# Performance work log

Hardware: AMD Instinct MI355X
Metric: run time of the kernel (lower is better)

The kernel has to match this reference:

```python
import jax, jax.numpy as jnp
import numpy as np

N = 100000   # nodes
E = 800000   # directed edges (before self-loops)
D = 64       # hidden_dim
NUM_ROUNDS = 4
EPS = 1e-5


def setup_inputs() -> dict:
    key = jax.random.key(0)
    k0, k1, k2 = jax.random.split(key, 3)
    x = jax.random.normal(k0, (N, D), dtype=jnp.float32)
    edge_index = jax.random.randint(k1, (2, E), 0, N, dtype=jnp.int32)
    W = jax.random.normal(k2, (D, D), dtype=jnp.float32) * (1.0 / np.sqrt(D))
    b = jnp.zeros((D,), dtype=jnp.float32)
    gamma = jnp.ones((D,), dtype=jnp.float32)
    beta = jnp.zeros((D,), dtype=jnp.float32)
    return {"x": x, "edge_index": edge_index, "W": W, "b": b,
            "gamma": gamma, "beta": beta, "num_rounds": NUM_ROUNDS}


def reference(x, edge_index, W, b, gamma, beta, num_rounds):
    n = x.shape[0]
    # GCNConv: add self-loops, symmetric degree normalization D^-1/2 (A+I) D^-1/2
    loops = jnp.arange(n, dtype=edge_index.dtype)
    src = jnp.concatenate([edge_index[0], loops])  # [E+N] message sources
    dst = jnp.concatenate([edge_index[1], loops])  # [E+N] message targets
    deg = jax.ops.segment_sum(jnp.ones_like(dst, dtype=x.dtype), dst, num_segments=n)
    dis = jnp.where(deg > 0, jax.lax.rsqrt(deg), 0.0)  # deg^-1/2, 0 for isolated
    norm = dis[src] * dis[dst]                          # [E+N] edge weights

    for _ in range(num_rounds):
        h = x @ W                                                      # [N, D]
        msgs = h[src] * norm[:, None]                                  # gather [E+N, D]
        agg = jax.ops.segment_sum(msgs, dst, num_segments=n) + b      # scatter-add
        # LayerNorm over feature dim
        mu = agg.mean(axis=-1, keepdims=True)
        var = agg.var(axis=-1, keepdims=True)
        x = (agg - mu) * jax.lax.rsqrt(var + EPS) * gamma + beta
    return x
```

## Files before the change

### kernel.cpp

```cpp
#include <hip/hip_runtime.h>

#define D 64
#define EPSV 1e-5f
#define SLOTP 16
#define SLOTS2 24
#define BSH 9
#define BNODES (1 << BSH)
#define BCAP 8192
#define SRCBITS 17
#define SRCMASK ((1u << SRCBITS) - 1)
#define DGSHIFT 26

typedef _Float16 f16;
typedef _Float16 f16x8 __attribute__((ext_vector_type(8)));
typedef float f32x4 __attribute__((ext_vector_type(4)));


__global__ void k_init(int* gcnt, int nbk, const float* __restrict__ W,
                       f16* __restrict__ Wp) {
    const int t = threadIdx.x;
    if (t < nbk) gcnt[t] = 0;
    for (int idx = t; idx < 512; idx += 256) {
        int s = idx >> 8, rem = idx & 255, tt = rem >> 6, l = rem & 63;
        int q = l >> 4, c = l & 15;
#pragma unroll
        for (int j = 0; j < 8; ++j) {
            int k = 32 * s + 8 * q + j;
            Wp[(size_t)idx * 8 + j] = (f16)W[k * D + 16 * tt + c];
        }
    }
}

__global__ __launch_bounds__(256) void k_binA(
    const int* __restrict__ src, const int* __restrict__ dst,
    int* __restrict__ gcnt, unsigned* __restrict__ breg, int e, int nbk) {
    __shared__ int bcnt[256];
    __shared__ int gbase[256];
    const int tid = threadIdx.x;
    if (tid < nbk) bcnt[tid] = 0;
    __syncthreads();

    const int per = (e + gridDim.x - 1) / gridDim.x;
    const int lo = blockIdx.x * per;
    const int hi = min(e, lo + per);

    for (int i = lo + tid; i < hi; i += 256)
        atomicAdd(&bcnt[dst[i] >> BSH], 1);
    __syncthreads();

    if (tid < nbk) {
        int c = bcnt[tid];
        gbase[tid] = (c > 0) ? atomicAdd(&gcnt[tid], c) : 0;
        bcnt[tid] = 0;
    }
    __syncthreads();

    for (int i = lo + tid; i < hi; i += 256) {
        int d_ = dst[i], s_ = src[i];
        int bkt = d_ >> BSH;
        int p = gbase[bkt] + atomicAdd(&bcnt[bkt], 1);
        if (p < BCAP)
            breg[(size_t)bkt * BCAP + p] =
                ((unsigned)(d_ & (BNODES - 1)) << SRCBITS) | (unsigned)s_;
    }
}

__global__ __launch_bounds__(256) void k_binB(
    const int* __restrict__ gcnt, const unsigned* __restrict__ breg,
    unsigned* __restrict__ slots, unsigned* __restrict__ slots2,
    const float* __restrict__ x, const f16* __restrict__ Wp,
    f16* __restrict__ h, int n) {
    __shared__ int scnt[BNODES];
    __shared__ unsigned sbuf[BNODES][SLOTP];
    const int tid = threadIdx.x;
    const int bkt = blockIdx.x;
    const int base = bkt << BSH;
    const int nloc = min(BNODES, n - base);

    for (int i = tid; i < BNODES; i += 256) {
        scnt[i] = 0;
        sbuf[i][0] = 0;
    }
    __syncthreads();

    const int cnt = min(gcnt[bkt], BCAP);
    const unsigned* reg = breg + (size_t)bkt * BCAP;
    for (int i = tid; i < cnt; i += 256) {
        unsigned v = reg[i];
        int ld = v >> SRCBITS;
        unsigned s = v & SRCMASK;
        int p = atomicAdd(&scnt[ld], 1);
        if (p < SLOTP) sbuf[ld][p] = s;
        else if (p < SLOTP + SLOTS2)
            slots2[(size_t)(base + ld) * SLOTS2 + (p - SLOTP)] = s;
    }
    __syncthreads();

    for (int i = tid; i < nloc * 4; i += 256) {
        int ld = i >> 2, part = i & 3;
        uint4 v = ((const uint4*)sbuf[ld])[part];
        if (part == 0) v.x |= (unsigned)min(scnt[ld], 63) << DGSHIFT;
        ((uint4*)(slots + (size_t)(base + ld) * SLOTP))[part] = v;
    }

    const int lane = tid & 63, wv = tid >> 6;
    const int q = lane >> 4, c = lane & 15;
    const f16x8* wp = (const f16x8*)Wp;
    f16x8 w0 = wp[0 * 64 + lane], w1 = wp[1 * 64 + lane];
    f16x8 w2 = wp[2 * 64 + lane], w3 = wp[3 * 64 + lane];
    f16x8 w4 = wp[4 * 64 + lane], w5 = wp[5 * 64 + lane];
    f16x8 w6 = wp[6 * 64 + lane], w7 = wp[7 * 64 + lane];

    for (int t = wv; t < 32; t += 4) {
        const int row0 = base + t * 16;
        if (row0 >= n) break;
        const int rA = (row0 + c < n) ? (row0 + c) : (n - 1);

        const float4* xr = (const float4*)(x + (size_t)rA * D);
        float4 u0 = xr[2 * q], u1 = xr[2 * q + 1];
        float4 u2 = xr[8 + 2 * q], u3 = xr[9 + 2 * q];
        f16x8 a0 = (f16x8){(f16)u0.x, (f16)u0.y, (f16)u0.z, (f16)u0.w,
                           (f16)u1.x, (f16)u1.y, (f16)u1.z, (f16)u1.w};
        f16x8 a1 = (f16x8){(f16)u2.x, (f16)u2.y, (f16)u2.z, (f16)u2.w,
                           (f16)u3.x, (f16)u3.y, (f16)u3.z, (f16)u3.w};

        f32x4 d0 = {0,0,0,0}, d1 = {0,0,0,0}, d2 = {0,0,0,0}, d3 = {0,0,0,0};
        d0 = __builtin_amdgcn_mfma_f32_16x16x32_f16(a0, w0, d0, 0, 0, 0);
        d1 = __builtin_amdgcn_mfma_f32_16x16x32_f16(a0, w1, d1, 0, 0, 0);
        d2 = __builtin_amdgcn_mfma_f32_16x16x32_f16(a0, w2, d2, 0, 0, 0);
        d3 = __builtin_amdgcn_mfma_f32_16x16x32_f16(a0, w3, d3, 0, 0, 0);
        d0 = __builtin_amdgcn_mfma_f32_16x16x32_f16(a1, w4, d0, 0, 0, 0);
        d1 = __builtin_amdgcn_mfma_f32_16x16x32_f16(a1, w5, d1, 0, 0, 0);
        d2 = __builtin_amdgcn_mfma_f32_16x16x32_f16(a1, w6, d2, 0, 0, 0);
        d3 = __builtin_amdgcn_mfma_f32_16x16x32_f16(a1, w7, d3, 0, 0, 0);

#pragma unroll
        for (int r = 0; r < 4; ++r) {
            int row = row0 + q * 4 + r;
            if (row < n) {
                float dvr = rsqrtf((float)(scnt[t * 16 + q * 4 + r] + 1));
                f16* hr = h + (size_t)row * D + c;
                hr[0]  = (f16)(d0[r] * dvr);
                hr[16] = (f16)(d1[r] * dvr);
                hr[32] = (f16)(d2[r] * dvr);
                hr[48] = (f16)(d3[r] * dvr);
            }
        }
    }
}

template<bool LAST>
__global__ __launch_bounds__(256, 8) void k_fuse(
    const f16* __restrict__ h, const unsigned* __restrict__ slots,
    const unsigned* __restrict__ slots2,
    const float* __restrict__ bb, const float* __restrict__ gamma,
    const float* __restrict__ beta, const f16* __restrict__ Wp,
    float* __restrict__ out, f16* __restrict__ hnext, int n,
    int sq, int sr) {
    __shared__ __align__(16) f16 ylds[32][72];
    __shared__ int dgs[32];

    const int xb = blockIdx.x & 7, kb = blockIdx.x >> 3;
    const int bid = (xb < sr ? xb * (sq + 1) : sr * (sq + 1) + (xb - sr) * sq) + kb;

    const int tid = threadIdx.x;
    const int grp = tid >> 3;
    const int fl  = tid & 7;
    const int w = bid * 32 + grp;
    const bool act = (w < n);

    if (act) {
        const int jb = w * SLOTP;

        float acc[8];
        {
            f16x8 sv = *(const f16x8*)(h + (size_t)w * D + fl * 8);
#pragma unroll
            for (int f = 0; f < 8; ++f) acc[f] = (float)sv[f];
        }

        uint4 s0 = *(const uint4*)(slots + jb);
        uint4 s1 = *(const uint4*)(slots + jb + 4);
        uint4 s2 = *(const uint4*)(slots + jb + 8);
        const int dg = (int)(s0.x >> DGSHIFT);
        if (!LAST && fl == 0) dgs[grp] = dg;
        const unsigned idx[12] = {s0.x & SRCMASK, s0.y, s0.z, s0.w,
                                  s1.x, s1.y, s1.z, s1.w,
                                  s2.x, s2.y, s2.z, s2.w};
        f16x8 v[12];
#pragma unroll
        for (int k = 0; k < 12; ++k) {
            unsigned u = (k < dg) ? idx[k] : 0u;
            v[k] = *(const f16x8*)(h + (size_t)u * D + fl * 8);
        }
#pragma unroll
        for (int k = 0; k < 12; ++k) {
            float m = (k < dg) ? 1.0f : 0.0f;
#pragma unroll
            for (int f = 0; f < 8; ++f) acc[f] += m * (float)v[k][f];
        }
        const int dgp = (dg < SLOTP) ? dg : SLOTP;
        if (dgp > 12) {
            uint4 sr4 = *(const uint4*)(slots + jb + 12);
            const unsigned uu[4] = {sr4.x, sr4.y, sr4.z, sr4.w};
#pragma unroll
            for (int k = 0; k < 4; ++k) {
                unsigned u = (12 + k < dgp) ? uu[k] : 0u;
                float m = (12 + k < dgp) ? 1.0f : 0.0f;
                f16x8 vv = *(const f16x8*)(h + (size_t)u * D + fl * 8);
#pragma unroll
                for (int f = 0; f < 8; ++f) acc[f] += m * (float)vv[f];
            }
        }
        if (dg > SLOTP) {
            const unsigned* r2 = slots2 + (size_t)w * SLOTS2;
            int dg2 = dg - SLOTP; if (dg2 > SLOTS2) dg2 = SLOTS2;
#pragma unroll
            for (int base = 0; base < SLOTS2; base += 4) {
                if (base < dg2) {
                    uint4 sr4 = *(const uint4*)(r2 + base);
                    const unsigned uu[4] = {sr4.x, sr4.y, sr4.z, sr4.w};
#pragma unroll
                    for (int k = 0; k < 4; ++k) {
                        unsigned u = (base + k < dg2) ? uu[k] : 0u;
                        float m = (base + k < dg2) ? 1.0f : 0.0f;
                        f16x8 vv = *(const f16x8*)(h + (size_t)u * D + fl * 8);
#pragma unroll
                        for (int f = 0; f < 8; ++f) acc[f] += m * (float)vv[f];
                    }
                }
            }
        }

        const float dv = rsqrtf((float)(dg + 1));
        const float4 b0 = ((const float4*)bb)[fl * 2],    b1 = ((const float4*)bb)[fl * 2 + 1];
        const float4 g0 = ((const float4*)gamma)[fl * 2], g1 = ((const float4*)gamma)[fl * 2 + 1];
        const float4 e0 = ((const float4*)beta)[fl * 2],  e1 = ((const float4*)beta)[fl * 2 + 1];
        const float bs[8] = {b0.x, b0.y, b0.z, b0.w, b1.x, b1.y, b1.z, b1.w};
        const float gs[8] = {g0.x, g0.y, g0.z, g0.w, g1.x, g1.y, g1.z, g1.w};
        const float es[8] = {e0.x, e0.y, e0.z, e0.w, e1.x, e1.y, e1.z, e1.w};

#pragma unroll
        for (int f = 0; f < 8; ++f) acc[f] = acc[f] * dv + bs[f];

        float s = 0.0f;
#pragma unroll
        for (int f = 0; f < 8; ++f) s += acc[f];
#pragma unroll
        for (int m = 1; m < 8; m <<= 1) s += __shfl_xor(s, m);
        float mu = s * (1.0f / 64.0f);
        float dd[8], qv = 0.0f;
#pragma unroll
        for (int f = 0; f < 8; ++f) { dd[f] = acc[f] - mu; qv += dd[f] * dd[f]; }
#pragma unroll
        for (int m = 1; m < 8; m <<= 1) qv += __shfl_xor(qv, m);
        float rstd = rsqrtf(qv * (1.0f / 64.0f) + EPSV);

        if (LAST) {
            float4 o0, o1;
            o0.x = dd[0] * rstd * gs[0] + es[0]; o0.y = dd[1] * rstd * gs[1] + es[1];
            o0.z = dd[2] * rstd * gs[2] + es[2]; o0.w = dd[3] * rstd * gs[3] + es[3];
            o1.x = dd[4] * rstd * gs[4] + es[4]; o1.y = dd[5] * rstd * gs[5] + es[5];
            o1.z = dd[6] * rstd * gs[6] + es[6]; o1.w = dd[7] * rstd * gs[7] + es[7];
            float4* orow = (float4*)(out + (size_t)w * D);
            orow[fl * 2] = o0; orow[fl * 2 + 1] = o1;
        } else {
            f16x8 yv;
#pragma unroll
            for (int f = 0; f < 8; ++f) yv[f] = (f16)(dd[f] * rstd * gs[f] + es[f]);
            *(f16x8*)(&ylds[grp][fl * 8]) = yv;
        }
    }
    if (LAST) return;

    __syncthreads();

    const int wv = tid >> 6;
    const int lane = tid & 63;
    const int q = lane >> 4, c = lane & 15;

    const f16x8* wp = (const f16x8*)Wp;
    f16x8 wlo = wp[wv * 64 + lane];
    f16x8 whi = wp[(4 + wv) * 64 + lane];

    const int row0 = bid * 32;
#pragma unroll
    for (int rt = 0; rt < 2; ++rt) {
        f16x8 a0 = *(const f16x8*)(&ylds[rt * 16 + c][q * 8]);
        f16x8 a1 = *(const f16x8*)(&ylds[rt * 16 + c][32 + q * 8]);
        f32x4 d = {0, 0, 0, 0};
        d = __builtin_amdgcn_mfma_f32_16x16x32_f16(a0, wlo, d, 0, 0, 0);
        d = __builtin_amdgcn_mfma_f32_16x16x32_f16(a1, whi, d, 0, 0, 0);

        const int rbase = row0 + rt * 16;
#pragma unroll
        for (int r = 0; r < 4; ++r) {
            int row = rbase + q * 4 + r;
            if (row < n) {
                float dvr = rsqrtf((float)(dgs[rt * 16 + q * 4 + r] + 1));
                hnext[(size_t)row * D + wv * 16 + c] = (f16)(d[r] * dvr);
            }
        }
    }
}


extern "C" void kernel_launch(void* const* d_in, const int* in_sizes, int n_in,
                              void* d_out, int out_size, void* d_ws, size_t ws_size,
                              hipStream_t stream) {
    const float* x0    = (const float*)d_in[0];
    const int*   ei    = (const int*)d_in[1];
    const float* W     = (const float*)d_in[2];
    const float* b     = (const float*)d_in[3];
    const float* gamma = (const float*)d_in[4];
    const float* beta  = (const float*)d_in[5];

    const int N = in_sizes[0] / D;
    const int E = in_sizes[1] / 2;
    const int* src = ei;
    const int* dst = ei + E;
    const int nbk = (N + BNODES - 1) >> BSH;

    char* ws = (char*)d_ws;
    size_t off = 0;
    auto alloc = [&](size_t bytes) {
        off = (off + 255) & ~(size_t)255;
        void* p = ws + off;
        off += bytes;
        return p;
    };
    unsigned* slots  = (unsigned*)alloc((size_t)N * SLOTP * 4);
    unsigned* slots2 = (unsigned*)alloc((size_t)N * SLOTS2 * 4);
    int*      gcnt   = (int*)alloc((size_t)nbk * 4);
    unsigned* breg   = (unsigned*)alloc((size_t)nbk * BCAP * 4);
    f16*      Wp     = (f16*)alloc(512 * 8 * 2);
    f16*      hA     = (f16*)alloc((size_t)N * D * 2);
    f16*      hB     = (f16*)alloc((size_t)N * D * 2);
    (void)ws_size;

    k_init<<<1, 256, 0, stream>>>(gcnt, nbk, W, Wp);
    k_binA<<<128, 256, 0, stream>>>(src, dst, gcnt, breg, E, nbk);
    k_binB<<<nbk, 256, 0, stream>>>(gcnt, breg, slots, slots2, x0, Wp, hA, N);

    float* out = (float*)d_out;
    const int GG = (N + 31) / 32;
    const int sq = GG / 8, sr = GG % 8;

    k_fuse<false><<<GG, 256, 0, stream>>>(hA, slots, slots2, b, gamma, beta,
                                          Wp, nullptr, hB, N, sq, sr);
    k_fuse<false><<<GG, 256, 0, stream>>>(hB, slots, slots2, b, gamma, beta,
                                          Wp, nullptr, hA, N, sq, sr);
    k_fuse<false><<<GG, 256, 0, stream>>>(hA, slots, slots2, b, gamma, beta,
                                          Wp, nullptr, hB, N, sq, sr);
    k_fuse<true><<<GG, 256, 0, stream>>>(hB, slots, slots2, b, gamma, beta,
                                         Wp, out, nullptr, N, sq, sr);
}
```

Baseline: 248.3 us.

## Split initial feature transform out of binning kernel into its own launch

The first x@W MFMA transform moves out of the per-bucket binning kernel (196 blocks) into a separate kernel that gives each wave one 16-row tile across many more blocks. The binning kernel now writes a per-node deg^-1/2 array that the new kernel reads. This is meant to expose more parallelism for the dense transform, at the cost of an extra launch and an extra global round trip for the degree scales. The occupancy hint of 8 on the fused kernel's launch bounds is also dropped, which changes how the compiler allocates registers.

```diff
diff --git a/kernel.cpp b/kernel.cpp
--- a/kernel.cpp
+++ b/kernel.cpp
@@ -68,8 +68,7 @@
 __global__ __launch_bounds__(256) void k_binB(
     const int* __restrict__ gcnt, const unsigned* __restrict__ breg,
     unsigned* __restrict__ slots, unsigned* __restrict__ slots2,
-    const float* __restrict__ x, const f16* __restrict__ Wp,
-    f16* __restrict__ h, int n) {
+    float* __restrict__ disv, int n) {
     __shared__ int scnt[BNODES];
     __shared__ unsigned sbuf[BNODES][SLOTP];
     const int tid = threadIdx.x;
@@ -102,55 +101,61 @@
         if (part == 0) v.x |= (unsigned)min(scnt[ld], 63) << DGSHIFT;
         ((uint4*)(slots + (size_t)(base + ld) * SLOTP))[part] = v;
     }
-
-    const int lane = tid & 63, wv = tid >> 6;
+    for (int i = tid; i < nloc; i += 256)
+        disv[base + i] = rsqrtf((float)(scnt[i] + 1));
+}
+
+__global__ __launch_bounds__(256) void k_xform(
+    const float* __restrict__ x, const f16* __restrict__ Wp,
+    const float* __restrict__ disv, f16* __restrict__ h, int n, int ntiles) {
+    const int tile = blockIdx.x * 4 + (threadIdx.x >> 6);
+    if (tile >= ntiles) return;
+    const int lane = threadIdx.x & 63;
     const int q = lane >> 4, c = lane & 15;
+
     const f16x8* wp = (const f16x8*)Wp;
     f16x8 w0 = wp[0 * 64 + lane], w1 = wp[1 * 64 + lane];
     f16x8 w2 = wp[2 * 64 + lane], w3 = wp[3 * 64 + lane];
     f16x8 w4 = wp[4 * 64 + lane], w5 = wp[5 * 64 + lane];
     f16x8 w6 = wp[6 * 64 + lane], w7 = wp[7 * 64 + lane];
 
-    for (int t = wv; t < 32; t += 4) {
-        const int row0 = base + t * 16;
-        if (row0 >= n) break;
-        const int rA = (row0 + c < n) ? (row0 + c) : (n - 1);
-
-        const float4* xr = (const float4*)(x + (size_t)rA * D);
-        float4 u0 = xr[2 * q], u1 = xr[2 * q + 1];
-        float4 u2 = xr[8 + 2 * q], u3 = xr[9 + 2 * q];
-        f16x8 a0 = (f16x8){(f16)u0.x, (f16)u0.y, (f16)u0.z, (f16)u0.w,
-                           (f16)u1.x, (f16)u1.y, (f16)u1.z, (f16)u1.w};
-        f16x8 a1 = (f16x8){(f16)u2.x, (f16)u2.y, (f16)u2.z, (f16)u2.w,
-                           (f16)u3.x, (f16)u3.y, (f16)u3.z, (f16)u3.w};
-
-        f32x4 d0 = {0,0,0,0}, d1 = {0,0,0,0}, d2 = {0,0,0,0}, d3 = {0,0,0,0};
-        d0 = __builtin_amdgcn_mfma_f32_16x16x32_f16(a0, w0, d0, 0, 0, 0);
-        d1 = __builtin_amdgcn_mfma_f32_16x16x32_f16(a0, w1, d1, 0, 0, 0);
-        d2 = __builtin_amdgcn_mfma_f32_16x16x32_f16(a0, w2, d2, 0, 0, 0);
-        d3 = __builtin_amdgcn_mfma_f32_16x16x32_f16(a0, w3, d3, 0, 0, 0);
-        d0 = __builtin_amdgcn_mfma_f32_16x16x32_f16(a1, w4, d0, 0, 0, 0);
-        d1 = __builtin_amdgcn_mfma_f32_16x16x32_f16(a1, w5, d1, 0, 0, 0);
-        d2 = __builtin_amdgcn_mfma_f32_16x16x32_f16(a1, w6, d2, 0, 0, 0);
-        d3 = __builtin_amdgcn_mfma_f32_16x16x32_f16(a1, w7, d3, 0, 0, 0);
-
-#pragma unroll
-        for (int r = 0; r < 4; ++r) {
-            int row = row0 + q * 4 + r;
-            if (row < n) {
-                float dvr = rsqrtf((float)(scnt[t * 16 + q * 4 + r] + 1));
-                f16* hr = h + (size_t)row * D + c;
-                hr[0]  = (f16)(d0[r] * dvr);
-                hr[16] = (f16)(d1[r] * dvr);
-                hr[32] = (f16)(d2[r] * dvr);
-                hr[48] = (f16)(d3[r] * dvr);
-            }
+    const int row0 = tile * 16;
+    const int rA = (row0 + c < n) ? (row0 + c) : (n - 1);
+
+    const float4* xr = (const float4*)(x + (size_t)rA * D);
+    float4 u0 = xr[2 * q], u1 = xr[2 * q + 1];
+    float4 u2 = xr[8 + 2 * q], u3 = xr[9 + 2 * q];
+    f16x8 a0 = (f16x8){(f16)u0.x, (f16)u0.y, (f16)u0.z, (f16)u0.w,
+                       (f16)u1.x, (f16)u1.y, (f16)u1.z, (f16)u1.w};
+    f16x8 a1 = (f16x8){(f16)u2.x, (f16)u2.y, (f16)u2.z, (f16)u2.w,
+                       (f16)u3.x, (f16)u3.y, (f16)u3.z, (f16)u3.w};
+
+    f32x4 d0 = {0,0,0,0}, d1 = {0,0,0,0}, d2 = {0,0,0,0}, d3 = {0,0,0,0};
+    d0 = __builtin_amdgcn_mfma_f32_16x16x32_f16(a0, w0, d0, 0, 0, 0);
+    d1 = __builtin_amdgcn_mfma_f32_16x16x32_f16(a0, w1, d1, 0, 0, 0);
+    d2 = __builtin_amdgcn_mfma_f32_16x16x32_f16(a0, w2, d2, 0, 0, 0);
+    d3 = __builtin_amdgcn_mfma_f32_16x16x32_f16(a0, w3, d3, 0, 0, 0);
+    d0 = __builtin_amdgcn_mfma_f32_16x16x32_f16(a1, w4, d0, 0, 0, 0);
+    d1 = __builtin_amdgcn_mfma_f32_16x16x32_f16(a1, w5, d1, 0, 0, 0);
+    d2 = __builtin_amdgcn_mfma_f32_16x16x32_f16(a1, w6, d2, 0, 0, 0);
+    d3 = __builtin_amdgcn_mfma_f32_16x16x32_f16(a1, w7, d3, 0, 0, 0);
+
+    f32x4 dvv = *(const f32x4*)(disv + row0 + 4 * q);
+#pragma unroll
+    for (int r = 0; r < 4; ++r) {
+        int row = row0 + q * 4 + r;
+        if (row < n) {
+            f16* hr = h + (size_t)row * D + c;
+            hr[0]  = (f16)(d0[r] * dvv[r]);
+            hr[16] = (f16)(d1[r] * dvv[r]);
+            hr[32] = (f16)(d2[r] * dvv[r]);
+            hr[48] = (f16)(d3[r] * dvv[r]);
         }
     }
 }
 
 template<bool LAST>
-__global__ __launch_bounds__(256, 8) void k_fuse(
+__global__ __launch_bounds__(256) void k_fuse(
     const f16* __restrict__ h, const unsigned* __restrict__ slots,
     const unsigned* __restrict__ slots2,
     const float* __restrict__ bb, const float* __restrict__ gamma,
@@ -333,6 +338,7 @@
     unsigned* slots2 = (unsigned*)alloc((size_t)N * SLOTS2 * 4);
     int*      gcnt   = (int*)alloc((size_t)nbk * 4);
     unsigned* breg   = (unsigned*)alloc((size_t)nbk * BCAP * 4);
+    float*    disv   = (float*)alloc((size_t)(N + 32) * 4);
     f16*      Wp     = (f16*)alloc(512 * 8 * 2);
     f16*      hA     = (f16*)alloc((size_t)N * D * 2);
     f16*      hB     = (f16*)alloc((size_t)N * D * 2);
@@ -340,12 +346,15 @@
 
     k_init<<<1, 256, 0, stream>>>(gcnt, nbk, W, Wp);
     k_binA<<<128, 256, 0, stream>>>(src, dst, gcnt, breg, E, nbk);
-    k_binB<<<nbk, 256, 0, stream>>>(gcnt, breg, slots, slots2, x0, Wp, hA, N);
+    k_binB<<<nbk, 256, 0, stream>>>(gcnt, breg, slots, slots2, disv, N);
 
     float* out = (float*)d_out;
+    const int ntiles = (N + 15) / 16;
+    const int GX = (ntiles + 3) / 4;
     const int GG = (N + 31) / 32;
     const int sq = GG / 8, sr = GG % 8;
 
+    k_xform<<<GX, 256, 0, stream>>>(x0, Wp, disv, hA, N, ntiles);
     k_fuse<false><<<GG, 256, 0, stream>>>(hA, slots, slots2, b, gamma, beta,
                                           Wp, nullptr, hB, N, sq, sr);
     k_fuse<false><<<GG, 256, 0, stream>>>(hB, slots, slots2, b, gamma, beta,
```

Result: faster. 215.4 us (-13.3%).
